# Kernel optimization log

Measured on AMD Instinct MI355X. Metric: run time of the kernel, lower is better.

Reference implementation:

```python
import jax, jax.numpy as jnp
import numpy as np

NUM_HEADS = 8
QKV_DIM = 32
DIM = 256
MULTI_Q = QKV_DIM * NUM_HEADS  # 256
BN_EPS = 1e-5


def conv1x1_bn(x, W, gamma, beta, mean, var):
    # 1x1 conv (no bias) followed by BatchNorm2d in eval mode.
    y = jnp.einsum('bchw,oc->bohw', x, W)
    inv = gamma / jnp.sqrt(var + BN_EPS)
    return y * inv[None, :, None, None] + (beta - mean * inv)[None, :, None, None]


def setup_inputs() -> dict:
    key = jax.random.key(0)
    ks = jax.random.split(key, 16)
    B, C, H, W = 16, DIM, 64, 64
    inp = {
        'input_': jax.random.normal(ks[0], (B, C, H, W), jnp.float32),
        'key_v_input_reduction': jax.random.normal(ks[1], (B, C, 32, 32), jnp.float32),
        # to_q: Conv2d_BN(dim -> multi_q_dim)
        'Wq': jax.random.normal(ks[2], (MULTI_Q, DIM), jnp.float32) * 0.05,
        'gq': jnp.ones((MULTI_Q,), jnp.float32),
        'bq': jnp.zeros((MULTI_Q,), jnp.float32),
        'mq': jax.random.normal(ks[3], (MULTI_Q,), jnp.float32) * 0.1,
        'vq': jax.random.uniform(ks[4], (MULTI_Q,), jnp.float32, 0.5, 1.5),
        # to_kv: Conv2d_BN(dim -> qkv_dim) (one_kv_head=True, share_kv=True)
        'Wkv': jax.random.normal(ks[5], (QKV_DIM, DIM), jnp.float32) * 0.05,
        'gkv': jnp.ones((QKV_DIM,), jnp.float32),
        'bkv': jnp.zeros((QKV_DIM,), jnp.float32),
        'mkv': jax.random.normal(ks[6], (QKV_DIM,), jnp.float32) * 0.1,
        'vkv': jax.random.uniform(ks[7], (QKV_DIM,), jnp.float32, 0.5, 1.5),
        # proj: activation -> Conv2d_BN(multi_q_dim -> dim)
        'Wp': jax.random.normal(ks[8], (DIM, MULTI_Q), jnp.float32) * 0.05,
        'gp': jnp.ones((DIM,), jnp.float32),
        'bp': jnp.zeros((DIM,), jnp.float32),
        'mp': jax.random.normal(ks[9], (DIM,), jnp.float32) * 0.1,
        'vp': jax.random.uniform(ks[10], (DIM,), jnp.float32, 0.5, 1.5),
    }
    return inp


def reference(input_, key_v_input_reduction, Wq, gq, bq, mq, vq,
              Wkv, gkv, bkv, mkv, vkv, Wp, gp, bp, mp, vp):
    B, C, H, W = input_.shape
    HW = H * W
    # Q projection -> (B, nh, d, HW)
    queries = conv1x1_bn(input_, Wq, gq, bq, mq, vq).reshape(B, NUM_HEADS, QKV_DIM, HW)
    # shared K=V projection, single kv head -> (B, 1, d, HW)
    kv = conv1x1_bn(input_, Wkv, gkv, bkv, mkv, vkv).reshape(B, 1, QKV_DIM, HW)
    key = jax.nn.softmax(kv, axis=3)       # softmax over spatial positions
    query = jax.nn.softmax(queries, axis=2)  # softmax over channel dim
    value = kv
    # context = key @ value^T : (B,1,d,d)
    context = jnp.einsum('bhdn,bhen->bhde', key, value)
    # permute(0,1,3,2) then broadcast over heads, attended = context^T @ query
    ctx_t = jnp.swapaxes(context, -1, -2)   # (B,1,d,d)
    attended = jnp.einsum('bhde,bken->bkdn'.replace('h', 'o'), ctx_t[:, 0][:, None], query) if False else jnp.matmul(ctx_t, query)  # (B,nh,d,HW) via broadcast
    attended = attended.reshape(B, MULTI_Q, H, W)
    # proj: ReLU then Conv2d_BN
    out = conv1x1_bn(jax.nn.relu(attended), Wp, gp, bp, mp, vp)
    return out
```

## Files before the change

kernel.cpp:

```cpp
#include <hip/hip_runtime.h>
#include <hip/hip_bf16.h>
#include <cstdint>

typedef _Float16 f16;
typedef _Float16 f16x4 __attribute__((ext_vector_type(4)));
typedef _Float16 f16x8 __attribute__((ext_vector_type(8)));
typedef float f32x4 __attribute__((ext_vector_type(4)));

#define MFMA16(a, b, c) __builtin_amdgcn_mfma_f32_16x16x32_f16((a), (b), (c), 0, 0, 0)

constexpr int BATCH = 16;
constexpr int C     = 256;
constexpr int HW    = 4096;
constexpr int DH    = 32;
constexpr float EPS = 1e-5f;

constexpr size_t OFF_XT = 0;
constexpr size_t SZ_XT  = (size_t)BATCH * HW * C * 2;
constexpr size_t OFF_KV = OFF_XT + SZ_XT;
constexpr size_t SZ_KV  = (size_t)BATCH * DH * HW * 4;
constexpr size_t OFF_W1 = OFF_KV + SZ_KV;
constexpr size_t OFF_B1 = OFF_W1 + 147456;
constexpr size_t OFF_WP = OFF_B1 + 2048;
constexpr size_t SZ_WP  = (size_t)C * C * 2;
constexpr size_t OFF_BP = OFF_WP + SZ_WP;
constexpr size_t OFF_U  = OFF_BP + 1024;
constexpr size_t OFF_PM = OFF_U + 65536;
constexpr size_t OFF_PS = OFF_PM + 131072;

__device__ __forceinline__ f16x8 ld8(const f16* p) {
  f16x4 lo = *(const f16x4*)p;
  f16x4 hi = *(const f16x4*)(p + 4);
  return __builtin_shufflevector(lo, hi, 0, 1, 2, 3, 4, 5, 6, 7);
}

__global__ __launch_bounds__(256) void k0_prep(
    const float* __restrict__ Wq,  const float* __restrict__ gq,  const float* __restrict__ bq,
    const float* __restrict__ mq,  const float* __restrict__ vq,
    const float* __restrict__ Wkv, const float* __restrict__ gkv, const float* __restrict__ bkv,
    const float* __restrict__ mkv, const float* __restrict__ vkv,
    const float* __restrict__ Wp,  const float* __restrict__ gp,  const float* __restrict__ bp,
    const float* __restrict__ mp,  const float* __restrict__ vp,
    f16* __restrict__ WqF, float* __restrict__ b1, f16* __restrict__ WpF,
    float* __restrict__ bp2, f16* __restrict__ WkvF, float* __restrict__ U) {
  int id = blockIdx.x * 256 + threadIdx.x;
  if (id < 65536) {
    int j = id & 7, lane = (id >> 3) & 63, ot = (id >> 9) & 15, kc = id >> 13;
    int o = ot * 16 + (lane & 15), c = kc * 32 + ((lane >> 4) << 3) + j;
    float inv = gq[o] * rsqrtf(vq[o] + EPS);
    WqF[id] = (f16)(Wq[o * 256 + c] * inv);
  } else if (id < 131072) {
    int id2 = id - 65536;
    int j = id2 & 7, lane = (id2 >> 3) & 63, ot = (id2 >> 9) & 15, kc = id2 >> 13;
    int o = ot * 16 + (lane & 15), c = kc * 32 + ((lane >> 4) << 3) + j;
    float inv = gp[o] * rsqrtf(vp[o] + EPS);
    WpF[id2] = (f16)(Wp[o * 256 + c] * inv);
  } else if (id < 139264) {
    int id2 = id - 131072;
    int j = id2 & 7, lane = (id2 >> 3) & 63, ot = (id2 >> 9) & 1, kc = id2 >> 10;
    int o = ot * 16 + (lane & 15), c = kc * 32 + ((lane >> 4) << 3) + j;
    float inv = gkv[o] * rsqrtf(vkv[o] + EPS);
    WkvF[id2] = (f16)(Wkv[o * 256 + c] * inv);
  } else if (id < 139552) {
    int r = id - 139264;
    if (r < 256) { float inv = gq[r] * rsqrtf(vq[r] + EPS);   b1[r] = bq[r] - mq[r] * inv; }
    else { int e = r - 256; float inv = gkv[e] * rsqrtf(vkv[e] + EPS); b1[r] = bkv[e] - mkv[e] * inv; }
  } else if (id < 139808) {
    int o = id - 139552;
    float inv = gp[o] * rsqrtf(vp[o] + EPS);
    bp2[o] = bp[o] - mp[o] * inv;
  } else if (id < 139808 + 16384) {
    U[id - 139808] = 0.f;
  }
}

__global__ __launch_bounds__(256, 4) void p0_trans_kv(
    const float* __restrict__ X, const f16* __restrict__ WkvF, const float* __restrict__ bkv1,
    f16* __restrict__ XTF, float* __restrict__ kvo,
    float* __restrict__ pmax, float* __restrict__ psum) {
  __shared__ alignas(16) f16 xt[64 * 260];
  float* kvb = (float*)xt;
  const int t = threadIdx.x, b = blockIdx.y, n0 = blockIdx.x * 64;
  const int lane = t & 63, w = t >> 6, l15 = lane & 15, quad = lane >> 4;
  const float* Xb = X + (size_t)b * C * HW;

  {
    int n4 = (t & 15) * 4, c4 = (t >> 4) * 4;
#pragma unroll
    for (int ci = 0; ci < 4; ++ci) {
      int c0 = ci * 64 + c4;
      const float* xp = Xb + (size_t)c0 * HW + n0 + n4;
      float4 v0 = *(const float4*)&xp[0];
      float4 v1 = *(const float4*)&xp[HW];
      float4 v2 = *(const float4*)&xp[2 * HW];
      float4 v3 = *(const float4*)&xp[3 * HW];
      f16x4 w0 = {(f16)v0.x, (f16)v1.x, (f16)v2.x, (f16)v3.x};
      f16x4 w1 = {(f16)v0.y, (f16)v1.y, (f16)v2.y, (f16)v3.y};
      f16x4 w2 = {(f16)v0.z, (f16)v1.z, (f16)v2.z, (f16)v3.z};
      f16x4 w3 = {(f16)v0.w, (f16)v1.w, (f16)v2.w, (f16)v3.w};
      *(f16x4*)&xt[(n4 + 0) * 260 + c0] = w0;
      *(f16x4*)&xt[(n4 + 1) * 260 + c0] = w1;
      *(f16x4*)&xt[(n4 + 2) * 260 + c0] = w2;
      *(f16x4*)&xt[(n4 + 3) * 260 + c0] = w3;
    }
  }
  __syncthreads();

  {
    f16* XFt = XTF + ((size_t)b * 64 + blockIdx.x) * 16384;
#pragma unroll
    for (int i = 0; i < 8; ++i) {
      int u = t + i * 256;
      int l15u = u & 15, qdu = (u >> 4) & 3, ntu = (u >> 6) & 3, kcu = u >> 8;
      f16x8 v = ld8(&xt[(ntu * 16 + l15u) * 260 + kcu * 32 + qdu * 8]);
      *(f16x8*)&XFt[(size_t)u * 8] = v;
    }
  }

  f32x4 acc0, acc1;
  {
    float bv0 = bkv1[l15], bv1 = bkv1[16 + l15];
#pragma unroll
    for (int r = 0; r < 4; ++r) { acc0[r] = bv0; acc1[r] = bv1; }
  }
#pragma unroll
  for (int kc = 0; kc < 8; ++kc) {
    f16x8 af  = ld8(&xt[(w * 16 + l15) * 260 + kc * 32 + quad * 8]);
    f16x8 bf0 = *(const f16x8*)&WkvF[((size_t)(kc * 2 + 0) * 64 + lane) * 8];
    f16x8 bf1 = *(const f16x8*)&WkvF[((size_t)(kc * 2 + 1) * 64 + lane) * 8];
    acc0 = MFMA16(af, bf0, acc0);
    acc1 = MFMA16(af, bf1, acc1);
  }
  __syncthreads();
#pragma unroll
  for (int r = 0; r < 4; ++r) {
    int n = w * 16 + quad * 4 + r;
    kvb[l15 * 68 + n] = acc0[r];
    kvb[(16 + l15) * 68 + n] = acc1[r];
  }
  __syncthreads();
#pragma unroll
  for (int i = 0; i < 2; ++i) {
    int u = t + i * 256, d = u >> 4, seg = u & 15;
    float4 v = *(const float4*)&kvb[d * 68 + seg * 4];
    *(float4*)&kvo[((size_t)b * DH + d) * HW + n0 + seg * 4] = v;
  }

  {
    int d = t >> 3, j = t & 7;
    float vals[8];
#pragma unroll
    for (int q = 0; q < 8; ++q) vals[q] = kvb[d * 68 + j * 8 + q];
    float m = vals[0];
#pragma unroll
    for (int q = 1; q < 8; ++q) m = fmaxf(m, vals[q]);
#pragma unroll
    for (int off = 1; off <= 4; off <<= 1) m = fmaxf(m, __shfl_xor(m, off));
    float s = 0.f;
#pragma unroll
    for (int q = 0; q < 8; ++q) s += __expf(vals[q] - m);
#pragma unroll
    for (int off = 1; off <= 4; off <<= 1) s += __shfl_xor(s, off);
    if (j == 0) {
      pmax[((size_t)b * DH + d) * 64 + blockIdx.x] = m;
      psum[((size_t)b * DH + d) * 64 + blockIdx.x] = s;
    }
  }
}

__global__ __launch_bounds__(256, 4) void k3_ctx(
    const float* __restrict__ kv, const float* __restrict__ pmax,
    const float* __restrict__ psum, float* __restrict__ U) {
  __shared__ float cacc[32 * 33];
  __shared__ float Ms[32], SiS[32];
  const int t = threadIdx.x, b = blockIdx.y;
  const int lane = t & 63, w = t >> 6, l15 = lane & 15, quad = lane >> 4;
  for (int i = t; i < 32 * 33; i += 256) cacc[i] = 0.f;

  {
    int i = t >> 3, j = t & 7;
    const float* pm = pmax + ((size_t)b * DH + i) * 64 + j * 8;
    const float* ps = psum + ((size_t)b * DH + i) * 64 + j * 8;
    float mv[8], sv[8];
#pragma unroll
    for (int q = 0; q < 8; ++q) { mv[q] = pm[q]; sv[q] = ps[q]; }
    float M = mv[0];
#pragma unroll
    for (int q = 1; q < 8; ++q) M = fmaxf(M, mv[q]);
#pragma unroll
    for (int off = 1; off <= 4; off <<= 1) M = fmaxf(M, __shfl_xor(M, off));
    float S = 0.f;
#pragma unroll
    for (int q = 0; q < 8; ++q) S += sv[q] * __expf(mv[q] - M);
#pragma unroll
    for (int off = 1; off <= 4; off <<= 1) S += __shfl_xor(S, off);
    if (j == 0) { Ms[i] = M; SiS[i] = 1.f / S; }
  }
  __syncthreads();

  const float* kvb = kv + (size_t)b * DH * HW;
  float M0 = Ms[l15],      Si0 = SiS[l15];
  float M1 = Ms[16 + l15], Si1 = SiS[16 + l15];
  f32x4 acc[2][2] = {};
#pragma unroll
  for (int s = 0; s < 2; ++s) {
    int nb = blockIdx.x * 256 + w * 64 + s * 32 + quad * 8;
    const float* p0 = &kvb[(size_t)l15 * HW + nb];
    const float* p1 = &kvb[(size_t)(16 + l15) * HW + nb];
    float lo[8], hi[8];
    *(float4*)&lo[0] = *(const float4*)&p0[0]; *(float4*)&lo[4] = *(const float4*)&p0[4];
    *(float4*)&hi[0] = *(const float4*)&p1[0]; *(float4*)&hi[4] = *(const float4*)&p1[4];
    f16x8 A0, A1, B0, B1;
#pragma unroll
    for (int j = 0; j < 8; ++j) {
      A0[j] = (f16)lo[j]; A1[j] = (f16)hi[j];
      B0[j] = (f16)(__expf(lo[j] - M0) * Si0);
      B1[j] = (f16)(__expf(hi[j] - M1) * Si1);
    }
    acc[0][0] = MFMA16(A0, B0, acc[0][0]);
    acc[1][0] = MFMA16(A1, B0, acc[1][0]);
    acc[0][1] = MFMA16(A0, B1, acc[0][1]);
    acc[1][1] = MFMA16(A1, B1, acc[1][1]);
  }
#pragma unroll
  for (int a = 0; a < 2; ++a)
#pragma unroll
    for (int e2 = 0; e2 < 2; ++e2)
#pragma unroll
      for (int r = 0; r < 4; ++r)
        atomicAdd(&cacc[(a * 16 + quad * 4 + r) * 33 + e2 * 16 + l15], acc[a][e2][r]);
  __syncthreads();
  for (int i = t; i < 1024; i += 256)
    atomicAdd(&U[b * 1024 + (i >> 5) * 32 + (i & 31)], cacc[(i >> 5) * 33 + (i & 31)]);
}

__global__ __launch_bounds__(256, 3) void kb_mega(
    const f16* __restrict__ XTF, const f16* __restrict__ WqF, const float* __restrict__ bq1,
    const float* __restrict__ U, const f16* __restrict__ WpF, const float* __restrict__ bp1,
    float* __restrict__ out) {
  __shared__ alignas(16) f16 pa[64 * 260];
  __shared__ alignas(16) f16 ctxs[32 * 36];
  const int t = threadIdx.x, b = blockIdx.y, n0 = blockIdx.x * 64;
  const int lane = t & 63, w = t >> 6, l15 = lane & 15, quad = lane >> 4;
  const int wn = w & 1, wm = w >> 1;

  {
    const float4 u4 = *(const float4*)&U[b * 1024 + t * 4];
    int d = t >> 3, e4 = (t & 7) * 4;
    f16x4 pk = {(f16)u4.x, (f16)u4.y, (f16)u4.z, (f16)u4.w};
    *(f16x4*)&ctxs[d * 36 + e4] = pk;
  }

  f32x4 acc1[2][8];
#pragma unroll
  for (int nf = 0; nf < 8; ++nf) {
    float bv = bq1[wn * 128 + nf * 16 + l15];
#pragma unroll
    for (int mf = 0; mf < 2; ++mf)
#pragma unroll
      for (int r = 0; r < 4; ++r) acc1[mf][nf][r] = bv;
  }
  {
    const f16* XF = XTF + ((size_t)b * 64 + blockIdx.x) * 16384;
    const f16* xb = XF + ((size_t)(wm * 2) * 64 + lane) * 8;
    const f16* wb = WqF + ((size_t)(wn * 8) * 64 + lane) * 8;
    f16x8 va0 = *(const f16x8*)&xb[0];
    f16x8 va1 = *(const f16x8*)&xb[512];
    f16x8 vw[8];
#pragma unroll
    for (int nf = 0; nf < 8; ++nf) vw[nf] = *(const f16x8*)&wb[nf * 512];
#pragma unroll 1
    for (int kc = 0; kc < 8; ++kc) {
      f16x8 na0, na1, nw[8];
      if (kc < 7) {
        const f16* xb2 = xb + (kc + 1) * 2048;
        const f16* wb2 = wb + (kc + 1) * 8192;
        na0 = *(const f16x8*)&xb2[0];
        na1 = *(const f16x8*)&xb2[512];
#pragma unroll
        for (int nf = 0; nf < 8; ++nf) nw[nf] = *(const f16x8*)&wb2[nf * 512];
      }
      __builtin_amdgcn_s_setprio(1);
#pragma unroll
      for (int nf = 0; nf < 8; ++nf) {
        acc1[0][nf] = MFMA16(va0, vw[nf], acc1[0][nf]);
        acc1[1][nf] = MFMA16(va1, vw[nf], acc1[1][nf]);
      }
      __builtin_amdgcn_s_setprio(0);
      va0 = na0; va1 = na1;
#pragma unroll
      for (int nf = 0; nf < 8; ++nf) vw[nf] = nw[nf];
    }
  }

#pragma unroll
  for (int mf = 0; mf < 2; ++mf)
#pragma unroll
    for (int h = 0; h < 4; ++h) {
      f32x4 v0 = acc1[mf][h * 2], v1 = acc1[mf][h * 2 + 1];
      f32x4 mx;
#pragma unroll
      for (int r = 0; r < 4; ++r) mx[r] = fmaxf(v0[r], v1[r]);
#pragma unroll
      for (int off = 1; off <= 8; off <<= 1)
#pragma unroll
        for (int r = 0; r < 4; ++r) mx[r] = fmaxf(mx[r], __shfl_xor(mx[r], off));
      f32x4 s4;
#pragma unroll
      for (int r = 0; r < 4; ++r) {
        v0[r] = __expf(v0[r] - mx[r]); v1[r] = __expf(v1[r] - mx[r]);
        s4[r] = v0[r] + v1[r];
      }
#pragma unroll
      for (int off = 1; off <= 8; off <<= 1)
#pragma unroll
        for (int r = 0; r < 4; ++r) s4[r] += __shfl_xor(s4[r], off);
      int o0 = wn * 128 + h * 32 + l15;
#pragma unroll
      for (int r = 0; r < 4; ++r) {
        int n = wm * 32 + mf * 16 + quad * 4 + r;
        float si = 1.f / s4[r];
        pa[n * 260 + o0]      = (f16)(v0[r] * si);
        pa[n * 260 + o0 + 16] = (f16)(v1[r] * si);
      }
    }
  __syncthreads();

  f32x4 datt[2][2][4] = {};
#pragma unroll
  for (int hh = 0; hh < 2; ++hh) {
    int h = w * 2 + hh;
#pragma unroll
    for (int mt = 0; mt < 2; ++mt) {
      f16x8 af = ld8(&ctxs[(mt * 16 + l15) * 36 + quad * 8]);
      __builtin_amdgcn_s_setprio(1);
#pragma unroll
      for (int nt = 0; nt < 4; ++nt) {
        f16x8 bf = ld8(&pa[(nt * 16 + l15) * 260 + h * 32 + quad * 8]);
        datt[hh][mt][nt] = MFMA16(af, bf, datt[hh][mt][nt]);
      }
      __builtin_amdgcn_s_setprio(0);
    }
  }
#pragma unroll
  for (int hh = 0; hh < 2; ++hh) {
    int h = w * 2 + hh;
#pragma unroll
    for (int mt = 0; mt < 2; ++mt)
#pragma unroll
      for (int nt = 0; nt < 4; ++nt)
#pragma unroll
        for (int r = 0; r < 4; ++r) {
          int n = nt * 16 + l15;
          int cc = h * 32 + mt * 16 + quad * 4 + r;
          pa[n * 260 + cc] = (f16)fmaxf(datt[hh][mt][nt][r], 0.f);
        }
  }
  __syncthreads();

  f32x4 acc2[8][2];
#pragma unroll
  for (int mf = 0; mf < 8; ++mf)
#pragma unroll
    for (int r = 0; r < 4; ++r) {
      float bv = bp1[wm * 128 + mf * 16 + quad * 4 + r];
      acc2[mf][0][r] = bv; acc2[mf][1][r] = bv;
    }
  {
    const f16* wb = WpF + ((size_t)(wm * 8) * 64 + lane) * 8;
    f16x8 vw[8];
#pragma unroll
    for (int mf = 0; mf < 8; ++mf) vw[mf] = *(const f16x8*)&wb[mf * 512];
#pragma unroll 1
    for (int kc = 0; kc < 8; ++kc) {
      f16x8 nw[8];
      if (kc < 7) {
        const f16* wb2 = wb + (kc + 1) * 8192;
#pragma unroll
        for (int mf = 0; mf < 8; ++mf) nw[mf] = *(const f16x8*)&wb2[mf * 512];
      }
      f16x8 bf0 = ld8(&pa[(wn * 32 + l15) * 260 + kc * 32 + quad * 8]);
      f16x8 bf1 = ld8(&pa[(wn * 32 + 16 + l15) * 260 + kc * 32 + quad * 8]);
      __builtin_amdgcn_s_setprio(1);
#pragma unroll
      for (int mf = 0; mf < 8; ++mf) {
        acc2[mf][0] = MFMA16(vw[mf], bf0, acc2[mf][0]);
        acc2[mf][1] = MFMA16(vw[mf], bf1, acc2[mf][1]);
      }
      __builtin_amdgcn_s_setprio(0);
#pragma unroll
      for (int mf = 0; mf < 8; ++mf) vw[mf] = nw[mf];
    }
  }
#pragma unroll
  for (int mf = 0; mf < 8; ++mf)
#pragma unroll
    for (int nf = 0; nf < 2; ++nf) {
      int n = n0 + wn * 32 + nf * 16 + l15;
#pragma unroll
      for (int r = 0; r < 4; ++r) {
        int o = wm * 128 + mf * 16 + quad * 4 + r;
        out[((size_t)b * C + o) * HW + n] = acc2[mf][nf][r];
      }
    }
}

extern "C" void kernel_launch(void* const* d_in, const int* in_sizes, int n_in,
                              void* d_out, int out_size, void* d_ws, size_t ws_size,
                              hipStream_t stream) {
  (void)in_sizes; (void)n_in; (void)out_size; (void)ws_size;
  const float* input = (const float*)d_in[0];
  const float* Wq  = (const float*)d_in[2];
  const float* gq  = (const float*)d_in[3];
  const float* bq  = (const float*)d_in[4];
  const float* mq  = (const float*)d_in[5];
  const float* vq  = (const float*)d_in[6];
  const float* Wkv = (const float*)d_in[7];
  const float* gkv = (const float*)d_in[8];
  const float* bkv = (const float*)d_in[9];
  const float* mkv = (const float*)d_in[10];
  const float* vkv = (const float*)d_in[11];
  const float* Wp  = (const float*)d_in[12];
  const float* gp  = (const float*)d_in[13];
  const float* bp  = (const float*)d_in[14];
  const float* mp  = (const float*)d_in[15];
  const float* vp  = (const float*)d_in[16];

  char* ws = (char*)d_ws;
  f16*   XTF = (f16*)(ws + OFF_XT);
  float* kvw = (float*)(ws + OFF_KV);
  f16*   WqF = (f16*)(ws + OFF_W1);
  f16*   WkvF= (f16*)(ws + OFF_W1 + 131072);
  float* b1  = (float*)(ws + OFF_B1);
  f16*   WpF = (f16*)(ws + OFF_WP);
  float* bp2 = (float*)(ws + OFF_BP);
  float* U   = (float*)(ws + OFF_U);
  float* pm  = (float*)(ws + OFF_PM);
  float* ps  = (float*)(ws + OFF_PS);
  float* out = (float*)d_out;

  const float* bq1  = b1;
  const float* bkv1 = b1 + 256;

  k0_prep<<<611, 256, 0, stream>>>(Wq, gq, bq, mq, vq, Wkv, gkv, bkv, mkv, vkv,
                                   Wp, gp, bp, mp, vp, WqF, b1, WpF, bp2, WkvF, U);
  p0_trans_kv<<<dim3(64, 16), 256, 0, stream>>>(input, WkvF, bkv1, XTF, kvw, pm, ps);
  k3_ctx<<<dim3(16, 16), 256, 0, stream>>>(kvw, pm, ps, U);
  kb_mega<<<dim3(64, 16), 256, 0, stream>>>(XTF, WqF, bq1, U, WpF, bp2, out);
}
```

Measured before the change: 203.6 us.

## Move Q projection and channel softmax into first pass, store softmaxed Q fragments

The Q projection GEMM and its per-head channel softmax move from the final kernel into the first pass. That pass already holds the transposed input tile in shared memory and now also computes the KV projection there. The first pass writes the softmaxed Q in MFMA fragment layout instead of the fp16 transposed input, so the final kernel loads those fragments straight into registers. The final kernel is left with context-apply, ReLU and output projection, and its occupancy hint rises from 3 to 4. The intermediate buffer keeps the same size, but the first pass gets heavier and the software prefetch of weights in the final kernel is dropped.

```diff
diff --git a/kernel.cpp b/kernel.cpp
--- a/kernel.cpp
+++ b/kernel.cpp
@@ -15,9 +15,9 @@
 constexpr int DH    = 32;
 constexpr float EPS = 1e-5f;
 
-constexpr size_t OFF_XT = 0;
-constexpr size_t SZ_XT  = (size_t)BATCH * HW * C * 2;
-constexpr size_t OFF_KV = OFF_XT + SZ_XT;
+constexpr size_t OFF_PF = 0;
+constexpr size_t SZ_PF  = (size_t)BATCH * HW * C * 2;
+constexpr size_t OFF_KV = OFF_PF + SZ_PF;
 constexpr size_t SZ_KV  = (size_t)BATCH * DH * HW * 4;
 constexpr size_t OFF_W1 = OFF_KV + SZ_KV;
 constexpr size_t OFF_B1 = OFF_W1 + 147456;
@@ -75,13 +75,16 @@
 }
 
 __global__ __launch_bounds__(256, 4) void p0_trans_kv(
-    const float* __restrict__ X, const f16* __restrict__ WkvF, const float* __restrict__ bkv1,
-    f16* __restrict__ XTF, float* __restrict__ kvo,
+    const float* __restrict__ X, const f16* __restrict__ WqF, const f16* __restrict__ WkvF,
+    const float* __restrict__ bq1, const float* __restrict__ bkv1,
+    f16* __restrict__ PF, float* __restrict__ kvo,
     float* __restrict__ pmax, float* __restrict__ psum) {
   __shared__ alignas(16) f16 xt[64 * 260];
+  f16* pa = xt;
   float* kvb = (float*)xt;
   const int t = threadIdx.x, b = blockIdx.y, n0 = blockIdx.x * 64;
   const int lane = t & 63, w = t >> 6, l15 = lane & 15, quad = lane >> 4;
+  const int wn = w & 1, wm = w >> 1;
   const float* Xb = X + (size_t)b * C * HW;
 
   {
@@ -106,46 +109,104 @@
   }
   __syncthreads();
 
-  {
-    f16* XFt = XTF + ((size_t)b * 64 + blockIdx.x) * 16384;
+  f32x4 acc1[2][8];
+  f32x4 acckv[2];
+#pragma unroll
+  for (int nf = 0; nf < 8; ++nf) {
+    float bv = bq1[wn * 128 + nf * 16 + l15];
+#pragma unroll
+    for (int mf = 0; mf < 2; ++mf)
+#pragma unroll
+      for (int r = 0; r < 4; ++r) acc1[mf][nf][r] = bv;
+  }
+  {
+    float bv = bkv1[wn * 16 + l15];
+#pragma unroll
+    for (int r = 0; r < 4; ++r) { acckv[0][r] = bv; acckv[1][r] = bv; }
+  }
+#pragma unroll 1
+  for (int kc = 0; kc < 8; ++kc) {
+    f16x8 a0 = ld8(&xt[(wm * 32 + l15) * 260 + kc * 32 + quad * 8]);
+    f16x8 a1 = ld8(&xt[(wm * 32 + 16 + l15) * 260 + kc * 32 + quad * 8]);
+    f16x8 bkvf = *(const f16x8*)&WkvF[((size_t)(kc * 2 + wn) * 64 + lane) * 8];
+    acckv[0] = MFMA16(a0, bkvf, acckv[0]);
+    acckv[1] = MFMA16(a1, bkvf, acckv[1]);
+#pragma unroll
+    for (int nf = 0; nf < 8; ++nf) {
+      f16x8 bf = *(const f16x8*)&WqF[((size_t)(kc * 16 + wn * 8 + nf) * 64 + lane) * 8];
+      acc1[0][nf] = MFMA16(a0, bf, acc1[0][nf]);
+      acc1[1][nf] = MFMA16(a1, bf, acc1[1][nf]);
+    }
+  }
+
+#pragma unroll
+  for (int mf = 0; mf < 2; ++mf)
+#pragma unroll
+    for (int h = 0; h < 4; ++h) {
+      f32x4 v0 = acc1[mf][h * 2], v1 = acc1[mf][h * 2 + 1];
+      f32x4 mx;
+#pragma unroll
+      for (int r = 0; r < 4; ++r) mx[r] = fmaxf(v0[r], v1[r]);
+#pragma unroll
+      for (int off = 1; off <= 8; off <<= 1)
+#pragma unroll
+        for (int r = 0; r < 4; ++r) mx[r] = fmaxf(mx[r], __shfl_xor(mx[r], off));
+      f32x4 s4;
+#pragma unroll
+      for (int r = 0; r < 4; ++r) {
+        v0[r] = __expf(v0[r] - mx[r]); v1[r] = __expf(v1[r] - mx[r]);
+        s4[r] = v0[r] + v1[r];
+      }
+#pragma unroll
+      for (int off = 1; off <= 8; off <<= 1)
+#pragma unroll
+        for (int r = 0; r < 4; ++r) s4[r] += __shfl_xor(s4[r], off);
+#pragma unroll
+      for (int r = 0; r < 4; ++r) {
+        float si = 1.f / s4[r];
+        v0[r] *= si; v1[r] *= si;
+      }
+      acc1[mf][h * 2] = v0; acc1[mf][h * 2 + 1] = v1;
+    }
+  __syncthreads();
+
+#pragma unroll
+  for (int mf = 0; mf < 2; ++mf)
+#pragma unroll
+    for (int nf = 0; nf < 8; ++nf)
+#pragma unroll
+      for (int r = 0; r < 4; ++r) {
+        int n = wm * 32 + mf * 16 + quad * 4 + r;
+        int o = wn * 128 + nf * 16 + l15;
+        pa[n * 260 + o] = (f16)acc1[mf][nf][r];
+      }
+  __syncthreads();
+
+  {
+    f16* PFt = PF + ((size_t)b * 64 + blockIdx.x) * 16384;
 #pragma unroll
     for (int i = 0; i < 8; ++i) {
       int u = t + i * 256;
-      int l15u = u & 15, qdu = (u >> 4) & 3, ntu = (u >> 6) & 3, kcu = u >> 8;
-      f16x8 v = ld8(&xt[(ntu * 16 + l15u) * 260 + kcu * 32 + qdu * 8]);
-      *(f16x8*)&XFt[(size_t)u * 8] = v;
-    }
-  }
-
-  f32x4 acc0, acc1;
-  {
-    float bv0 = bkv1[l15], bv1 = bkv1[16 + l15];
-#pragma unroll
-    for (int r = 0; r < 4; ++r) { acc0[r] = bv0; acc1[r] = bv1; }
-  }
-#pragma unroll
-  for (int kc = 0; kc < 8; ++kc) {
-    f16x8 af  = ld8(&xt[(w * 16 + l15) * 260 + kc * 32 + quad * 8]);
-    f16x8 bf0 = *(const f16x8*)&WkvF[((size_t)(kc * 2 + 0) * 64 + lane) * 8];
-    f16x8 bf1 = *(const f16x8*)&WkvF[((size_t)(kc * 2 + 1) * 64 + lane) * 8];
-    acc0 = MFMA16(af, bf0, acc0);
-    acc1 = MFMA16(af, bf1, acc1);
-  }
-  __syncthreads();
+      int lu = u & 63, ntu = (u >> 6) & 3, hu = u >> 8;
+      f16x8 v = ld8(&pa[(ntu * 16 + (lu & 15)) * 260 + hu * 32 + ((lu >> 4) << 3)]);
+      *(f16x8*)&PFt[(size_t)u * 8] = v;
+    }
+  }
+  __syncthreads();
+
 #pragma unroll
   for (int r = 0; r < 4; ++r) {
-    int n = w * 16 + quad * 4 + r;
-    kvb[l15 * 68 + n] = acc0[r];
-    kvb[(16 + l15) * 68 + n] = acc1[r];
-  }
-  __syncthreads();
+    kvb[(wn * 16 + l15) * 68 + wm * 32 + quad * 4 + r]      = acckv[0][r];
+    kvb[(wn * 16 + l15) * 68 + wm * 32 + 16 + quad * 4 + r] = acckv[1][r];
+  }
+  __syncthreads();
+
 #pragma unroll
   for (int i = 0; i < 2; ++i) {
     int u = t + i * 256, d = u >> 4, seg = u & 15;
     float4 v = *(const float4*)&kvb[d * 68 + seg * 4];
     *(float4*)&kvo[((size_t)b * DH + d) * HW + n0 + seg * 4] = v;
   }
-
   {
     int d = t >> 3, j = t & 7;
     float vals[8];
@@ -234,9 +295,9 @@
     atomicAdd(&U[b * 1024 + (i >> 5) * 32 + (i & 31)], cacc[(i >> 5) * 33 + (i & 31)]);
 }
 
-__global__ __launch_bounds__(256, 3) void kb_mega(
-    const f16* __restrict__ XTF, const f16* __restrict__ WqF, const float* __restrict__ bq1,
-    const float* __restrict__ U, const f16* __restrict__ WpF, const float* __restrict__ bp1,
+__global__ __launch_bounds__(256, 4) void kb_mega(
+    const f16* __restrict__ PF, const float* __restrict__ U,
+    const f16* __restrict__ WpF, const float* __restrict__ bp1,
     float* __restrict__ out) {
   __shared__ alignas(16) f16 pa[64 * 260];
   __shared__ alignas(16) f16 ctxs[32 * 36];
@@ -244,104 +305,35 @@
   const int lane = t & 63, w = t >> 6, l15 = lane & 15, quad = lane >> 4;
   const int wn = w & 1, wm = w >> 1;
 
+  f16x8 bfp[2][4];
+  {
+    const f16* PFt = PF + ((size_t)b * 64 + blockIdx.x) * 16384;
+#pragma unroll
+    for (int hh = 0; hh < 2; ++hh)
+#pragma unroll
+      for (int nt = 0; nt < 4; ++nt)
+        bfp[hh][nt] = *(const f16x8*)&PFt[(((size_t)(w * 2 + hh) * 4 + nt) * 64 + lane) * 8];
+  }
   {
     const float4 u4 = *(const float4*)&U[b * 1024 + t * 4];
     int d = t >> 3, e4 = (t & 7) * 4;
     f16x4 pk = {(f16)u4.x, (f16)u4.y, (f16)u4.z, (f16)u4.w};
     *(f16x4*)&ctxs[d * 36 + e4] = pk;
   }
-
-  f32x4 acc1[2][8];
-#pragma unroll
-  for (int nf = 0; nf < 8; ++nf) {
-    float bv = bq1[wn * 128 + nf * 16 + l15];
-#pragma unroll
-    for (int mf = 0; mf < 2; ++mf)
-#pragma unroll
-      for (int r = 0; r < 4; ++r) acc1[mf][nf][r] = bv;
-  }
-  {
-    const f16* XF = XTF + ((size_t)b * 64 + blockIdx.x) * 16384;
-    const f16* xb = XF + ((size_t)(wm * 2) * 64 + lane) * 8;
-    const f16* wb = WqF + ((size_t)(wn * 8) * 64 + lane) * 8;
-    f16x8 va0 = *(const f16x8*)&xb[0];
-    f16x8 va1 = *(const f16x8*)&xb[512];
-    f16x8 vw[8];
-#pragma unroll
-    for (int nf = 0; nf < 8; ++nf) vw[nf] = *(const f16x8*)&wb[nf * 512];
-#pragma unroll 1
-    for (int kc = 0; kc < 8; ++kc) {
-      f16x8 na0, na1, nw[8];
-      if (kc < 7) {
-        const f16* xb2 = xb + (kc + 1) * 2048;
-        const f16* wb2 = wb + (kc + 1) * 8192;
-        na0 = *(const f16x8*)&xb2[0];
-        na1 = *(const f16x8*)&xb2[512];
-#pragma unroll
-        for (int nf = 0; nf < 8; ++nf) nw[nf] = *(const f16x8*)&wb2[nf * 512];
-      }
-      __builtin_amdgcn_s_setprio(1);
-#pragma unroll
-      for (int nf = 0; nf < 8; ++nf) {
-        acc1[0][nf] = MFMA16(va0, vw[nf], acc1[0][nf]);
-        acc1[1][nf] = MFMA16(va1, vw[nf], acc1[1][nf]);
-      }
-      __builtin_amdgcn_s_setprio(0);
-      va0 = na0; va1 = na1;
-#pragma unroll
-      for (int nf = 0; nf < 8; ++nf) vw[nf] = nw[nf];
-    }
-  }
-
-#pragma unroll
-  for (int mf = 0; mf < 2; ++mf)
-#pragma unroll
-    for (int h = 0; h < 4; ++h) {
-      f32x4 v0 = acc1[mf][h * 2], v1 = acc1[mf][h * 2 + 1];
-      f32x4 mx;
-#pragma unroll
-      for (int r = 0; r < 4; ++r) mx[r] = fmaxf(v0[r], v1[r]);
-#pragma unroll
-      for (int off = 1; off <= 8; off <<= 1)
-#pragma unroll
-        for (int r = 0; r < 4; ++r) mx[r] = fmaxf(mx[r], __shfl_xor(mx[r], off));
-      f32x4 s4;
-#pragma unroll
-      for (int r = 0; r < 4; ++r) {
-        v0[r] = __expf(v0[r] - mx[r]); v1[r] = __expf(v1[r] - mx[r]);
-        s4[r] = v0[r] + v1[r];
-      }
-#pragma unroll
-      for (int off = 1; off <= 8; off <<= 1)
-#pragma unroll
-        for (int r = 0; r < 4; ++r) s4[r] += __shfl_xor(s4[r], off);
-      int o0 = wn * 128 + h * 32 + l15;
-#pragma unroll
-      for (int r = 0; r < 4; ++r) {
-        int n = wm * 32 + mf * 16 + quad * 4 + r;
-        float si = 1.f / s4[r];
-        pa[n * 260 + o0]      = (f16)(v0[r] * si);
-        pa[n * 260 + o0 + 16] = (f16)(v1[r] * si);
-      }
-    }
   __syncthreads();
 
   f32x4 datt[2][2][4] = {};
 #pragma unroll
-  for (int hh = 0; hh < 2; ++hh) {
-    int h = w * 2 + hh;
+  for (int hh = 0; hh < 2; ++hh)
 #pragma unroll
     for (int mt = 0; mt < 2; ++mt) {
       f16x8 af = ld8(&ctxs[(mt * 16 + l15) * 36 + quad * 8]);
       __builtin_amdgcn_s_setprio(1);
 #pragma unroll
-      for (int nt = 0; nt < 4; ++nt) {
-        f16x8 bf = ld8(&pa[(nt * 16 + l15) * 260 + h * 32 + quad * 8]);
-        datt[hh][mt][nt] = MFMA16(af, bf, datt[hh][mt][nt]);
-      }
+      for (int nt = 0; nt < 4; ++nt)
+        datt[hh][mt][nt] = MFMA16(af, bfp[hh][nt], datt[hh][mt][nt]);
       __builtin_amdgcn_s_setprio(0);
     }
-  }
 #pragma unroll
   for (int hh = 0; hh < 2; ++hh) {
     int h = w * 2 + hh;
@@ -366,31 +358,18 @@
       float bv = bp1[wm * 128 + mf * 16 + quad * 4 + r];
       acc2[mf][0][r] = bv; acc2[mf][1][r] = bv;
     }
-  {
-    const f16* wb = WpF + ((size_t)(wm * 8) * 64 + lane) * 8;
-    f16x8 vw[8];
-#pragma unroll
-    for (int mf = 0; mf < 8; ++mf) vw[mf] = *(const f16x8*)&wb[mf * 512];
 #pragma unroll 1
-    for (int kc = 0; kc < 8; ++kc) {
-      f16x8 nw[8];
-      if (kc < 7) {
-        const f16* wb2 = wb + (kc + 1) * 8192;
-#pragma unroll
-        for (int mf = 0; mf < 8; ++mf) nw[mf] = *(const f16x8*)&wb2[mf * 512];
-      }
-      f16x8 bf0 = ld8(&pa[(wn * 32 + l15) * 260 + kc * 32 + quad * 8]);
-      f16x8 bf1 = ld8(&pa[(wn * 32 + 16 + l15) * 260 + kc * 32 + quad * 8]);
-      __builtin_amdgcn_s_setprio(1);
-#pragma unroll
-      for (int mf = 0; mf < 8; ++mf) {
-        acc2[mf][0] = MFMA16(vw[mf], bf0, acc2[mf][0]);
-        acc2[mf][1] = MFMA16(vw[mf], bf1, acc2[mf][1]);
-      }
-      __builtin_amdgcn_s_setprio(0);
-#pragma unroll
-      for (int mf = 0; mf < 8; ++mf) vw[mf] = nw[mf];
-    }
+  for (int kc = 0; kc < 8; ++kc) {
+    f16x8 bf0 = ld8(&pa[(wn * 32 + l15) * 260 + kc * 32 + quad * 8]);
+    f16x8 bf1 = ld8(&pa[(wn * 32 + 16 + l15) * 260 + kc * 32 + quad * 8]);
+    __builtin_amdgcn_s_setprio(1);
+#pragma unroll
+    for (int mf = 0; mf < 8; ++mf) {
+      f16x8 af = *(const f16x8*)&WpF[((size_t)(kc * 16 + wm * 8 + mf) * 64 + lane) * 8];
+      acc2[mf][0] = MFMA16(af, bf0, acc2[mf][0]);
+      acc2[mf][1] = MFMA16(af, bf1, acc2[mf][1]);
+    }
+    __builtin_amdgcn_s_setprio(0);
   }
 #pragma unroll
   for (int mf = 0; mf < 8; ++mf)
@@ -427,7 +406,7 @@
   const float* vp  = (const float*)d_in[16];
 
   char* ws = (char*)d_ws;
-  f16*   XTF = (f16*)(ws + OFF_XT);
+  f16*   PFw = (f16*)(ws + OFF_PF);
   float* kvw = (float*)(ws + OFF_KV);
   f16*   WqF = (f16*)(ws + OFF_W1);
   f16*   WkvF= (f16*)(ws + OFF_W1 + 131072);
@@ -444,7 +423,8 @@
 
   k0_prep<<<611, 256, 0, stream>>>(Wq, gq, bq, mq, vq, Wkv, gkv, bkv, mkv, vkv,
                                    Wp, gp, bp, mp, vp, WqF, b1, WpF, bp2, WkvF, U);
-  p0_trans_kv<<<dim3(64, 16), 256, 0, stream>>>(input, WkvF, bkv1, XTF, kvw, pm, ps);
+  p0_trans_kv<<<dim3(64, 16), 256, 0, stream>>>(input, WqF, WkvF, bq1, bkv1,
+                                                PFw, kvw, pm, ps);
   k3_ctx<<<dim3(16, 16), 256, 0, stream>>>(kvw, pm, ps, U);
-  kb_mega<<<dim3(64, 16), 256, 0, stream>>>(XTF, WqF, bq1, U, WpF, bp2, out);
-}
+  kb_mega<<<dim3(64, 16), 256, 0, stream>>>(PFw, U, WpF, bp2, out);
+}
```

New measurement: 205.3 us. About the same (+0.8%).

## Fuse context computation into KV kernel using unnormalized exp and atomics

Applied to the files above, without the earlier changes.

The separate context kernel and the global kv buffer are removed. The KV projection kernel now computes each tile's partial exp(kv)·kv^T contribution with an MFMA and atomically adds it into U, and accumulates the softmax denominators into S. Normalization is deferred to the final kernel, which divides U by S when loading context. This saves a launch and an 8MB write/read round trip. In exchange it adds global atomic contention and drops the max-subtraction, so large kv values could overflow.

```diff
diff --git a/kernel.cpp b/kernel.cpp
--- a/kernel.cpp
+++ b/kernel.cpp
@@ -17,16 +17,13 @@
 
 constexpr size_t OFF_XT = 0;
 constexpr size_t SZ_XT  = (size_t)BATCH * HW * C * 2;
-constexpr size_t OFF_KV = OFF_XT + SZ_XT;
-constexpr size_t SZ_KV  = (size_t)BATCH * DH * HW * 4;
-constexpr size_t OFF_W1 = OFF_KV + SZ_KV;
+constexpr size_t OFF_W1 = OFF_XT + SZ_XT;
 constexpr size_t OFF_B1 = OFF_W1 + 147456;
 constexpr size_t OFF_WP = OFF_B1 + 2048;
 constexpr size_t SZ_WP  = (size_t)C * C * 2;
 constexpr size_t OFF_BP = OFF_WP + SZ_WP;
 constexpr size_t OFF_U  = OFF_BP + 1024;
-constexpr size_t OFF_PM = OFF_U + 65536;
-constexpr size_t OFF_PS = OFF_PM + 131072;
+constexpr size_t OFF_S  = OFF_U + 65536;
 
 __device__ __forceinline__ f16x8 ld8(const f16* p) {
   f16x4 lo = *(const f16x4*)p;
@@ -42,7 +39,8 @@
     const float* __restrict__ Wp,  const float* __restrict__ gp,  const float* __restrict__ bp,
     const float* __restrict__ mp,  const float* __restrict__ vp,
     f16* __restrict__ WqF, float* __restrict__ b1, f16* __restrict__ WpF,
-    float* __restrict__ bp2, f16* __restrict__ WkvF, float* __restrict__ U) {
+    float* __restrict__ bp2, f16* __restrict__ WkvF, float* __restrict__ U,
+    float* __restrict__ S) {
   int id = blockIdx.x * 256 + threadIdx.x;
   if (id < 65536) {
     int j = id & 7, lane = (id >> 3) & 63, ot = (id >> 9) & 15, kc = id >> 13;
@@ -69,19 +67,21 @@
     int o = id - 139552;
     float inv = gp[o] * rsqrtf(vp[o] + EPS);
     bp2[o] = bp[o] - mp[o] * inv;
-  } else if (id < 139808 + 16384) {
+  } else if (id < 156192) {
     U[id - 139808] = 0.f;
-  }
-}
-
-__global__ __launch_bounds__(256, 4) void p0_trans_kv(
+  } else if (id < 156704) {
+    S[id - 156192] = 0.f;
+  }
+}
+
+__global__ __launch_bounds__(256, 4) void ka_trans_kv(
     const float* __restrict__ X, const f16* __restrict__ WkvF, const float* __restrict__ bkv1,
-    f16* __restrict__ XTF, float* __restrict__ kvo,
-    float* __restrict__ pmax, float* __restrict__ psum) {
+    f16* __restrict__ XTF, float* __restrict__ U, float* __restrict__ S) {
   __shared__ alignas(16) f16 xt[64 * 260];
   float* kvb = (float*)xt;
   const int t = threadIdx.x, b = blockIdx.y, n0 = blockIdx.x * 64;
   const int lane = t & 63, w = t >> 6, l15 = lane & 15, quad = lane >> 4;
+  const int wn = w & 1, wm = w >> 1;
   const float* Xb = X + (size_t)b * C * HW;
 
   {
@@ -132,111 +132,48 @@
     acc1 = MFMA16(af, bf1, acc1);
   }
   __syncthreads();
+
 #pragma unroll
   for (int r = 0; r < 4; ++r) {
     int n = w * 16 + quad * 4 + r;
-    kvb[l15 * 68 + n] = acc0[r];
-    kvb[(16 + l15) * 68 + n] = acc1[r];
-  }
-  __syncthreads();
-#pragma unroll
-  for (int i = 0; i < 2; ++i) {
-    int u = t + i * 256, d = u >> 4, seg = u & 15;
-    float4 v = *(const float4*)&kvb[d * 68 + seg * 4];
-    *(float4*)&kvo[((size_t)b * DH + d) * HW + n0 + seg * 4] = v;
-  }
-
+    kvb[l15 * 65 + n] = acc0[r];
+    kvb[(16 + l15) * 65 + n] = acc1[r];
+  }
+  __syncthreads();
+
+  {
+    f32x4 cx = {0.f, 0.f, 0.f, 0.f};
+#pragma unroll
+    for (int ks = 0; ks < 2; ++ks) {
+      f16x8 A, B;
+#pragma unroll
+      for (int j = 0; j < 8; ++j) {
+        float av = kvb[(wn * 16 + l15) * 65 + ks * 32 + quad * 8 + j];
+        float bv = kvb[(wm * 16 + l15) * 65 + ks * 32 + quad * 8 + j];
+        A[j] = (f16)av;
+        B[j] = (f16)__expf(bv);
+      }
+      cx = MFMA16(A, B, cx);
+    }
+#pragma unroll
+    for (int r = 0; r < 4; ++r)
+      atomicAdd(&U[b * 1024 + (wn * 16 + quad * 4 + r) * 32 + wm * 16 + l15], cx[r]);
+  }
   {
     int d = t >> 3, j = t & 7;
-    float vals[8];
-#pragma unroll
-    for (int q = 0; q < 8; ++q) vals[q] = kvb[d * 68 + j * 8 + q];
-    float m = vals[0];
-#pragma unroll
-    for (int q = 1; q < 8; ++q) m = fmaxf(m, vals[q]);
-#pragma unroll
-    for (int off = 1; off <= 4; off <<= 1) m = fmaxf(m, __shfl_xor(m, off));
     float s = 0.f;
 #pragma unroll
-    for (int q = 0; q < 8; ++q) s += __expf(vals[q] - m);
+    for (int q = 0; q < 8; ++q) s += __expf(kvb[d * 65 + j * 8 + q]);
 #pragma unroll
     for (int off = 1; off <= 4; off <<= 1) s += __shfl_xor(s, off);
-    if (j == 0) {
-      pmax[((size_t)b * DH + d) * 64 + blockIdx.x] = m;
-      psum[((size_t)b * DH + d) * 64 + blockIdx.x] = s;
-    }
-  }
-}
-
-__global__ __launch_bounds__(256, 4) void k3_ctx(
-    const float* __restrict__ kv, const float* __restrict__ pmax,
-    const float* __restrict__ psum, float* __restrict__ U) {
-  __shared__ float cacc[32 * 33];
-  __shared__ float Ms[32], SiS[32];
-  const int t = threadIdx.x, b = blockIdx.y;
-  const int lane = t & 63, w = t >> 6, l15 = lane & 15, quad = lane >> 4;
-  for (int i = t; i < 32 * 33; i += 256) cacc[i] = 0.f;
-
-  {
-    int i = t >> 3, j = t & 7;
-    const float* pm = pmax + ((size_t)b * DH + i) * 64 + j * 8;
-    const float* ps = psum + ((size_t)b * DH + i) * 64 + j * 8;
-    float mv[8], sv[8];
-#pragma unroll
-    for (int q = 0; q < 8; ++q) { mv[q] = pm[q]; sv[q] = ps[q]; }
-    float M = mv[0];
-#pragma unroll
-    for (int q = 1; q < 8; ++q) M = fmaxf(M, mv[q]);
-#pragma unroll
-    for (int off = 1; off <= 4; off <<= 1) M = fmaxf(M, __shfl_xor(M, off));
-    float S = 0.f;
-#pragma unroll
-    for (int q = 0; q < 8; ++q) S += sv[q] * __expf(mv[q] - M);
-#pragma unroll
-    for (int off = 1; off <= 4; off <<= 1) S += __shfl_xor(S, off);
-    if (j == 0) { Ms[i] = M; SiS[i] = 1.f / S; }
-  }
-  __syncthreads();
-
-  const float* kvb = kv + (size_t)b * DH * HW;
-  float M0 = Ms[l15],      Si0 = SiS[l15];
-  float M1 = Ms[16 + l15], Si1 = SiS[16 + l15];
-  f32x4 acc[2][2] = {};
-#pragma unroll
-  for (int s = 0; s < 2; ++s) {
-    int nb = blockIdx.x * 256 + w * 64 + s * 32 + quad * 8;
-    const float* p0 = &kvb[(size_t)l15 * HW + nb];
-    const float* p1 = &kvb[(size_t)(16 + l15) * HW + nb];
-    float lo[8], hi[8];
-    *(float4*)&lo[0] = *(const float4*)&p0[0]; *(float4*)&lo[4] = *(const float4*)&p0[4];
-    *(float4*)&hi[0] = *(const float4*)&p1[0]; *(float4*)&hi[4] = *(const float4*)&p1[4];
-    f16x8 A0, A1, B0, B1;
-#pragma unroll
-    for (int j = 0; j < 8; ++j) {
-      A0[j] = (f16)lo[j]; A1[j] = (f16)hi[j];
-      B0[j] = (f16)(__expf(lo[j] - M0) * Si0);
-      B1[j] = (f16)(__expf(hi[j] - M1) * Si1);
-    }
-    acc[0][0] = MFMA16(A0, B0, acc[0][0]);
-    acc[1][0] = MFMA16(A1, B0, acc[1][0]);
-    acc[0][1] = MFMA16(A0, B1, acc[0][1]);
-    acc[1][1] = MFMA16(A1, B1, acc[1][1]);
-  }
-#pragma unroll
-  for (int a = 0; a < 2; ++a)
-#pragma unroll
-    for (int e2 = 0; e2 < 2; ++e2)
-#pragma unroll
-      for (int r = 0; r < 4; ++r)
-        atomicAdd(&cacc[(a * 16 + quad * 4 + r) * 33 + e2 * 16 + l15], acc[a][e2][r]);
-  __syncthreads();
-  for (int i = t; i < 1024; i += 256)
-    atomicAdd(&U[b * 1024 + (i >> 5) * 32 + (i & 31)], cacc[(i >> 5) * 33 + (i & 31)]);
+    if (j == 0) atomicAdd(&S[b * 32 + d], s);
+  }
 }
 
 __global__ __launch_bounds__(256, 3) void kb_mega(
     const f16* __restrict__ XTF, const f16* __restrict__ WqF, const float* __restrict__ bq1,
-    const float* __restrict__ U, const f16* __restrict__ WpF, const float* __restrict__ bp1,
+    const float* __restrict__ U, const float* __restrict__ S,
+    const f16* __restrict__ WpF, const float* __restrict__ bp1,
     float* __restrict__ out) {
   __shared__ alignas(16) f16 pa[64 * 260];
   __shared__ alignas(16) f16 ctxs[32 * 36];
@@ -247,7 +184,9 @@
   {
     const float4 u4 = *(const float4*)&U[b * 1024 + t * 4];
     int d = t >> 3, e4 = (t & 7) * 4;
-    f16x4 pk = {(f16)u4.x, (f16)u4.y, (f16)u4.z, (f16)u4.w};
+    const float4 s4 = *(const float4*)&S[b * 32 + e4];
+    f16x4 pk = {(f16)(u4.x / s4.x), (f16)(u4.y / s4.y),
+                (f16)(u4.z / s4.z), (f16)(u4.w / s4.w)};
     *(f16x4*)&ctxs[d * 36 + e4] = pk;
   }
 
@@ -375,7 +314,7 @@
     for (int kc = 0; kc < 8; ++kc) {
       f16x8 nw[8];
       if (kc < 7) {
-        const f16* wb2 = wb + (kc + 1) * 8192;
+        const f16* wb2 = wb + (size_t)(kc + 1) * 8192;
 #pragma unroll
         for (int mf = 0; mf < 8; ++mf) nw[mf] = *(const f16x8*)&wb2[mf * 512];
       }
@@ -428,23 +367,20 @@
 
   char* ws = (char*)d_ws;
   f16*   XTF = (f16*)(ws + OFF_XT);
-  float* kvw = (float*)(ws + OFF_KV);
   f16*   WqF = (f16*)(ws + OFF_W1);
   f16*   WkvF= (f16*)(ws + OFF_W1 + 131072);
   float* b1  = (float*)(ws + OFF_B1);
   f16*   WpF = (f16*)(ws + OFF_WP);
   float* bp2 = (float*)(ws + OFF_BP);
   float* U   = (float*)(ws + OFF_U);
-  float* pm  = (float*)(ws + OFF_PM);
-  float* ps  = (float*)(ws + OFF_PS);
+  float* S   = (float*)(ws + OFF_S);
   float* out = (float*)d_out;
 
   const float* bq1  = b1;
   const float* bkv1 = b1 + 256;
 
-  k0_prep<<<611, 256, 0, stream>>>(Wq, gq, bq, mq, vq, Wkv, gkv, bkv, mkv, vkv,
-                                   Wp, gp, bp, mp, vp, WqF, b1, WpF, bp2, WkvF, U);
-  p0_trans_kv<<<dim3(64, 16), 256, 0, stream>>>(input, WkvF, bkv1, XTF, kvw, pm, ps);
-  k3_ctx<<<dim3(16, 16), 256, 0, stream>>>(kvw, pm, ps, U);
-  kb_mega<<<dim3(64, 16), 256, 0, stream>>>(XTF, WqF, bq1, U, WpF, bp2, out);
-}
+  k0_prep<<<613, 256, 0, stream>>>(Wq, gq, bq, mq, vq, Wkv, gkv, bkv, mkv, vkv,
+                                   Wp, gp, bp, mp, vp, WqF, b1, WpF, bp2, WkvF, U, S);
+  ka_trans_kv<<<dim3(64, 16), 256, 0, stream>>>(input, WkvF, bkv1, XTF, U, S);
+  kb_mega<<<dim3(64, 16), 256, 0, stream>>>(XTF, WqF, bq1, U, S, WpF, bp2, out);
+}
```

Result: faster. 193.6 us (-4.9%).
